# Kernel tuning notes

Measured on AMD Instinct MI355X. Metric: run time of the kernel, lower is better.

Reference implementation:

```python
import jax, jax.numpy as jnp
import numpy as np

P, L, E, D, NL, FF = 1024, 32, 512, 768, 6, 3072
H_PA, H_TR = 4, 8
VOCAB = 256


def layer_norm(x, w, b, eps=1e-5):
    mu = x.mean(-1, keepdims=True)
    var = ((x - mu) ** 2).mean(-1, keepdims=True)
    return (x - mu) / jnp.sqrt(var + eps) * w + b


def mha(x, wqkv, bqkv, wo, bo, nheads, key_mask=None):
    # x: [B,S,E]; torch nn.MultiheadAttention semantics (scale q by 1/sqrt(d))
    B, S, Emb = x.shape
    d = Emb // nheads
    qkv = x @ wqkv.T + bqkv
    q, k, v = jnp.split(qkv, 3, axis=-1)
    hd = lambda t: t.reshape(B, S, nheads, d).transpose(0, 2, 1, 3)
    q, k, v = hd(q) * (d ** -0.5), hd(k), hd(v)
    scores = jnp.einsum('bhqd,bhkd->bhqk', q, k)
    if key_mask is not None:
        scores = jnp.where(key_mask[:, None, None, :], scores, -1e9)
    a = jax.nn.softmax(scores, axis=-1)
    o = jnp.einsum('bhqk,bhkd->bhqd', a, v).transpose(0, 2, 1, 3).reshape(B, S, Emb)
    return o @ wo.T + bo


def setup_inputs() -> dict:
    key = jax.random.key(0)
    ks = jax.random.split(key, 32)
    n = lambda i, shape, s=0.02: (jax.random.normal(ks[i], shape, dtype=jnp.float32) * s)
    x = lambda i, shape: jax.random.normal(ks[i], shape, dtype=jnp.float32) * (1.0 / np.sqrt(shape[-1]))
    tokens = jax.random.randint(ks[0], (P, L), 0, VOCAB, dtype=jnp.int32)
    lengths = jax.random.randint(ks[1], (P,), 4, L + 1, dtype=jnp.int32)
    byte_emb = n(2, (VOCAB, E)).at[0].set(0.0)  # padding_idx=0
    inp = {
        'tokens': tokens, 'lengths': lengths,
        'byte_emb': byte_emb,
        'local_pos_emb': n(3, (L, E)),
        'patch_pos_emb': n(4, (P, D)),
        'pa_qkv_w': x(5, (3 * E, E)), 'pa_qkv_b': jnp.zeros((3 * E,), jnp.float32),
        'pa_out_w': x(6, (E, E)), 'pa_out_b': jnp.zeros((E,), jnp.float32),
        'proj_w': x(7, (D, E)), 'proj_b': jnp.zeros((D,), jnp.float32),
        'layers_qkv_w': x(8, (NL, 3 * D, D)), 'layers_qkv_b': jnp.zeros((NL, 3 * D), jnp.float32),
        'layers_out_w': x(9, (NL, D, D)), 'layers_out_b': jnp.zeros((NL, D), jnp.float32),
        'layers_ln1_w': jnp.ones((NL, D), jnp.float32), 'layers_ln1_b': jnp.zeros((NL, D), jnp.float32),
        'layers_ln2_w': jnp.ones((NL, D), jnp.float32), 'layers_ln2_b': jnp.zeros((NL, D), jnp.float32),
        'layers_ff1_w': x(10, (NL, FF, D)), 'layers_ff1_b': jnp.zeros((NL, FF), jnp.float32),
        'layers_ff2_w': x(11, (NL, D, FF)), 'layers_ff2_b': jnp.zeros((NL, D), jnp.float32),
        'ln_f_w': jnp.ones((D,), jnp.float32), 'ln_f_b': jnp.zeros((D,), jnp.float32),
    }
    return inp


def reference(tokens, lengths, byte_emb, local_pos_emb, patch_pos_emb,
              pa_qkv_w, pa_qkv_b, pa_out_w, pa_out_b, proj_w, proj_b,
              layers_qkv_w, layers_qkv_b, layers_out_w, layers_out_b,
              layers_ln1_w, layers_ln1_b, layers_ln2_w, layers_ln2_b,
              layers_ff1_w, layers_ff1_b, layers_ff2_w, layers_ff2_b,
              ln_f_w, ln_f_b):
    mask = jnp.arange(L) < lengths[:, None]  # [P,L] valid-byte mask
    # encode_patches: byte embed + local positions, zero padded slots
    emb = byte_emb[tokens] + local_pos_emb[None, :, :]  # [P,L,E]
    emb = emb * mask[..., None].astype(emb.dtype)
    # per-patch MHA over bytes (key padding mask), vectorized across patches
    attn = mha(emb, pa_qkv_w, pa_qkv_b, pa_out_w, pa_out_b, H_PA, key_mask=mask)
    cnt = mask.sum(-1, keepdims=True).astype(emb.dtype)
    patch_repr = (attn * mask[..., None].astype(emb.dtype)).sum(1) / cnt  # [P,E] masked mean
    # project to hidden and add patch-level positions
    h = patch_repr @ proj_w.T + proj_b + patch_pos_emb[:P]
    h = h[None]  # [1,P,D]
    # pre-norm transformer encoder, gelu FFN
    for i in range(NL):
        hn = layer_norm(h, layers_ln1_w[i], layers_ln1_b[i])
        h = h + mha(hn, layers_qkv_w[i], layers_qkv_b[i], layers_out_w[i], layers_out_b[i], H_TR)
        hn = layer_norm(h, layers_ln2_w[i], layers_ln2_b[i])
        ff = jax.nn.gelu(hn @ layers_ff1_w[i].T + layers_ff1_b[i], approximate=False)
        h = h + ff @ layers_ff2_w[i].T + layers_ff2_b[i]
    return layer_norm(h, ln_f_w, ln_f_b)[0]  # [P,D]
```

## Files before the change

### kernel.cpp

```cpp
#include <hip/hip_runtime.h>
#include <hip/hip_bf16.h>
#include <math.h>

typedef __hip_bfloat16 bf16;
typedef unsigned short u16;
typedef __attribute__((ext_vector_type(8))) short short8;
typedef __attribute__((ext_vector_type(4))) float f32x4;

#define PP 1024
#define LL 32
#define EE 512
#define DD 768
#define NLAYER 6
#define FFDIM 3072

__device__ __forceinline__ float bf2f(u16 u) { return __uint_as_float(((unsigned)u) << 16); }
__device__ __forceinline__ u16 f2b(float x) {
  unsigned u = __float_as_uint(x);
  return (u16)((u + 0x7FFFu + ((u >> 16) & 1u)) >> 16);
}

__global__ __launch_bounds__(256) void cvt4(
    const float* s0, const float* s1, const float* s2, const float* s3,
    u16* d0, u16* d1, u16* d2, u16* d3,
    int n0, int n1, int n2, int n3)
{
  int r = blockIdx.y;
  const float* s = r == 0 ? s0 : r == 1 ? s1 : r == 2 ? s2 : s3;
  u16* d        = r == 0 ? d0 : r == 1 ? d1 : r == 2 ? d2 : d3;
  int n4        = r == 0 ? n0 : r == 1 ? n1 : r == 2 ? n2 : n3;
  int i = blockIdx.x * 256 + threadIdx.x;
  if (i < n4) {
    float4 v = ((const float4*)s)[i];
    ushort4 o;
    o.x = f2b(v.x); o.y = f2b(v.y); o.z = f2b(v.z); o.w = f2b(v.w);
    ((ushort4*)d)[i] = o;
  }
}

template<bool AEMB>
__global__ __launch_bounds__(256) void gemm64(
    const bf16* A, long sAb, int lda,
    const bf16* B, long sBb, int ldb,
    float* Cf, bf16* Cb, long sCb, int ldc,
    const float* bias, int biasStride,
    const float* addf,
    int M, int N, int K, int act,
    const int* tokens, const int* lengths,
    const float* be, const float* lp)
{
  __shared__ u16 As[2][64][72];
  __shared__ u16 Bs[2][64][72];
  const int bz = blockIdx.z;
  const u16* Ap = (const u16*)A + (long)bz * sAb;
  const u16* Bp = (const u16*)B + (long)bz * sBb;
  const long coff = (long)bz * sCb;
  const int m0 = blockIdx.x << 6, n0 = blockIdx.y << 6;
  const int tid = threadIdx.x;
  const int wave = tid >> 6, lane = tid & 63;
  const int sr = tid >> 3;
  const int scc = (tid & 7) << 3;
  const int br0 = n0 + sr, br1 = n0 + sr + 32;
  const short8 zz = {0,0,0,0,0,0,0,0};
  f32x4 acc[4] = {{0.f,0.f,0.f,0.f},{0.f,0.f,0.f,0.f},{0.f,0.f,0.f,0.f},{0.f,0.f,0.f,0.f}};

#define LOADA(row, kk, dest)                                                   \
  do {                                                                         \
    if (!AEMB) {                                                               \
      dest = *(const short8*)(Ap + (long)(row) * lda + (kk));                  \
    } else {                                                                   \
      int rr = (row); int ll = rr & 31;                                        \
      if (ll < lengths[rr >> 5]) {                                             \
        const float* bpp = be + ((long)tokens[rr] << 9) + (kk);                \
        const float* lpp = lp + ((long)ll << 9) + (kk);                        \
        float4 x0 = *(const float4*)bpp, x1 = *(const float4*)(bpp + 4);       \
        float4 y0 = *(const float4*)lpp, y1 = *(const float4*)(lpp + 4);       \
        dest[0] = (short)f2b(x0.x + y0.x); dest[1] = (short)f2b(x0.y + y0.y);  \
        dest[2] = (short)f2b(x0.z + y0.z); dest[3] = (short)f2b(x0.w + y0.w);  \
        dest[4] = (short)f2b(x1.x + y1.x); dest[5] = (short)f2b(x1.y + y1.y);  \
        dest[6] = (short)f2b(x1.z + y1.z); dest[7] = (short)f2b(x1.w + y1.w);  \
      } else dest = zz;                                                        \
    }                                                                          \
  } while (0)

  {
    int ch = K < 64 ? K : 64;
    bool kv = scc < ch;
    short8 a0 = zz, a1 = zz, b0 = zz, b1 = zz;
    if (kv) {
      LOADA(m0 + sr, scc, a0);
      LOADA(m0 + sr + 32, scc, a1);
      if (br0 < N) b0 = *(const short8*)(Bp + (long)br0 * ldb + scc);
      if (br1 < N) b1 = *(const short8*)(Bp + (long)br1 * ldb + scc);
    }
    *(short8*)&As[0][sr][scc] = a0;
    *(short8*)&As[0][sr + 32][scc] = a1;
    *(short8*)&Bs[0][sr][scc] = b0;
    *(short8*)&Bs[0][sr + 32][scc] = b1;
  }
  __syncthreads();

  const int arow = (wave << 4) + (lane & 15);
  const int kq = (lane >> 4) << 3;
  int buf = 0;
  for (int k0 = 0; k0 < K; k0 += 64) {
    int knext = k0 + 64;
    bool more = knext < K;
    short8 a0 = zz, a1 = zz, b0 = zz, b1 = zz;
    if (more) {
      int ch = K - knext; if (ch > 64) ch = 64;
      bool kv = scc < ch;
      if (kv) {
        LOADA(m0 + sr, knext + scc, a0);
        LOADA(m0 + sr + 32, knext + scc, a1);
        if (br0 < N) b0 = *(const short8*)(Bp + (long)br0 * ldb + knext + scc);
        if (br1 < N) b1 = *(const short8*)(Bp + (long)br1 * ldb + knext + scc);
      }
    }
    int rem = K - k0; if (rem > 64) rem = 64;
    {
      short8 af = *(const short8*)&As[buf][arow][kq];
#pragma unroll
      for (int nt = 0; nt < 4; nt++) {
        short8 bfr = *(const short8*)&Bs[buf][(nt << 4) + (lane & 15)][kq];
        acc[nt] = __builtin_amdgcn_mfma_f32_16x16x32_bf16(af, bfr, acc[nt], 0, 0, 0);
      }
    }
    if (rem > 32) {
      short8 af = *(const short8*)&As[buf][arow][32 + kq];
#pragma unroll
      for (int nt = 0; nt < 4; nt++) {
        short8 bfr = *(const short8*)&Bs[buf][(nt << 4) + (lane & 15)][32 + kq];
        acc[nt] = __builtin_amdgcn_mfma_f32_16x16x32_bf16(af, bfr, acc[nt], 0, 0, 0);
      }
    }
    if (more) {
      int nb = buf ^ 1;
      *(short8*)&As[nb][sr][scc] = a0;
      *(short8*)&As[nb][sr + 32][scc] = a1;
      *(short8*)&Bs[nb][sr][scc] = b0;
      *(short8*)&Bs[nb][sr + 32][scc] = b1;
      __syncthreads();
      buf = nb;
    }
  }
#undef LOADA

  int rbase = m0 + (wave << 4) + ((lane >> 4) << 2);
#pragma unroll
  for (int nt = 0; nt < 4; nt++) {
    int c = n0 + (nt << 4) + (lane & 15);
    if (c >= N) continue;
    float bvl = bias ? bias[bz * biasStride + c] : 0.f;
#pragma unroll
    for (int j = 0; j < 4; j++) {
      int r = rbase + j;
      long idx = coff + (long)r * ldc + c;
      float v = acc[nt][j] + bvl;
      if (addf) v += addf[idx];
      if (act == 1) v = 0.5f * v * (1.f + erff(v * 0.70710678118654752f));
      if (Cf) Cf[idx] = v;
      if (Cb) Cb[idx] = __float2bfloat16(v);
    }
  }
}

__global__ __launch_bounds__(256) void patch_attn(
    const bf16* __restrict__ qk,
    const int* __restrict__ tokens, const int* __restrict__ lengths,
    const float* __restrict__ byte_emb, const float* __restrict__ local_pos,
    bf16* __restrict__ Z)
{
  __shared__ float wsum[4][32];
  __shared__ int tok_s[32];
  __shared__ int cnt_s;
  int p = blockIdx.x;
  int tid = threadIdx.x;
  if (tid < 32) tok_s[tid] = tokens[p * 32 + tid];
  if (tid == 0) cnt_s = lengths[p];
  __syncthreads();
  int cnt = cnt_s;
  int h = tid >> 6, lane = tid & 63;
  const u16* base = (const u16*)qk + (long)p * 32 * 1024 + h * 128;
  const int rsel = lane & 15;
  const int ksel = (lane >> 4) << 3;

  f32x4 acc[2][2] = {{{0.f,0.f,0.f,0.f},{0.f,0.f,0.f,0.f}},
                     {{0.f,0.f,0.f,0.f},{0.f,0.f,0.f,0.f}}};
#pragma unroll
  for (int kc = 0; kc < 4; kc++) {
    int ko = kc * 32 + ksel;
    short8 a0 = *(const short8*)(base + (long)rsel * 1024 + ko);
    short8 a1 = *(const short8*)(base + (long)(16 + rsel) * 1024 + ko);
    short8 b0 = *(const short8*)(base + 512 + (long)rsel * 1024 + ko);
    short8 b1 = *(const short8*)(base + 512 + (long)(16 + rsel) * 1024 + ko);
    acc[0][0] = __builtin_amdgcn_mfma_f32_16x16x32_bf16(a0, b0, acc[0][0], 0, 0, 0);
    acc[0][1] = __builtin_amdgcn_mfma_f32_16x16x32_bf16(a0, b1, acc[0][1], 0, 0, 0);
    acc[1][0] = __builtin_amdgcn_mfma_f32_16x16x32_bf16(a1, b0, acc[1][0], 0, 0, 0);
    acc[1][1] = __builtin_amdgcn_mfma_f32_16x16x32_bf16(a1, b1, acc[1][1], 0, 0, 0);
  }

  const float scale = 0.088388347648318447f;
  int j0 = lane & 15, j1 = 16 + j0;
  bool v0 = j0 < cnt, v1 = j1 < cnt;
  int rowq = (lane >> 4) << 2;
  float cs0 = 0.f, cs1 = 0.f;
#pragma unroll
  for (int ti = 0; ti < 2; ti++) {
    float s0[4], s1[4], mx[4], sm[4], e0[4], e1[4];
#pragma unroll
    for (int r = 0; r < 4; r++) {
      s0[r] = acc[ti][0][r] * scale;
      s1[r] = acc[ti][1][r] * scale;
      float a = v0 ? s0[r] : -1e30f;
      float b = v1 ? s1[r] : -1e30f;
      mx[r] = fmaxf(a, b);
    }
#pragma unroll
    for (int d = 1; d < 16; d <<= 1)
#pragma unroll
      for (int r = 0; r < 4; r++) mx[r] = fmaxf(mx[r], __shfl_xor(mx[r], d));
#pragma unroll
    for (int r = 0; r < 4; r++) {
      e0[r] = v0 ? __expf(s0[r] - mx[r]) : 0.f;
      e1[r] = v1 ? __expf(s1[r] - mx[r]) : 0.f;
      sm[r] = e0[r] + e1[r];
    }
#pragma unroll
    for (int d = 1; d < 16; d <<= 1)
#pragma unroll
      for (int r = 0; r < 4; r++) sm[r] += __shfl_xor(sm[r], d);
#pragma unroll
    for (int r = 0; r < 4; r++) {
      int row = ti * 16 + rowq + r;
      if (row < cnt) {
        float inv = 1.f / sm[r];
        cs0 += e0[r] * inv;
        cs1 += e1[r] * inv;
      }
    }
  }
  cs0 += __shfl_xor(cs0, 16); cs0 += __shfl_xor(cs0, 32);
  cs1 += __shfl_xor(cs1, 16); cs1 += __shfl_xor(cs1, 32);
  if (lane < 16) {
    float invc = 1.f / (float)cnt;
    wsum[h][lane] = cs0 * invc;
    wsum[h][16 + lane] = cs1 * invc;
  }
  __syncthreads();

  for (int e = tid; e < 512; e += 256) {
    float za0 = 0.f, za1 = 0.f, za2 = 0.f, za3 = 0.f;
    for (int j = 0; j < cnt; j++) {
      float ev = byte_emb[((long)tok_s[j] << 9) + e] + local_pos[((long)j << 9) + e];
      za0 += wsum[0][j] * ev;
      za1 += wsum[1][j] * ev;
      za2 += wsum[2][j] * ev;
      za3 += wsum[3][j] * ev;
    }
    long zb = (long)p * 2048;
    Z[zb + e]        = __float2bfloat16(za0);
    Z[zb + 512 + e]  = __float2bfloat16(za1);
    Z[zb + 1024 + e] = __float2bfloat16(za2);
    Z[zb + 1536 + e] = __float2bfloat16(za3);
  }
}

__global__ __launch_bounds__(256) void ln_kernel(
    const float* __restrict__ x, const float* __restrict__ w, const float* __restrict__ b,
    bf16* outb, float* outf, int N)
{
  __shared__ float red[8];
  __shared__ float mv[2];
  int row = blockIdx.x;
  const float* xr = x + (long)row * N;
  int tid = threadIdx.x, lane = tid & 63, wave = tid >> 6;
  float s = 0.f, s2 = 0.f;
  for (int c = tid; c < N; c += 256) { float v = xr[c]; s += v; s2 += v * v; }
  for (int o = 32; o; o >>= 1) { s += __shfl_down(s, o); s2 += __shfl_down(s2, o); }
  if (lane == 0) { red[wave] = s; red[4 + wave] = s2; }
  __syncthreads();
  if (tid == 0) {
    float ts = red[0] + red[1] + red[2] + red[3];
    float ts2 = red[4] + red[5] + red[6] + red[7];
    float mu = ts / N;
    float var = ts2 / N - mu * mu;
    mv[0] = mu; mv[1] = rsqrtf(var + 1e-5f);
  }
  __syncthreads();
  float mu = mv[0], rstd = mv[1];
  for (int c = tid; c < N; c += 256) {
    float v = (xr[c] - mu) * rstd * w[c] + b[c];
    if (outb) outb[(long)row * N + c] = __float2bfloat16(v);
    if (outf) outf[(long)row * N + c] = v;
  }
}

__global__ __launch_bounds__(256) void softmax_bf(u16* __restrict__ S)
{
  __shared__ float red[4], red2[4];
  long row = blockIdx.x;
  u16* sr = S + row * 1024;
  int tid = threadIdx.x, lane = tid & 63, wave = tid >> 6;
  const float scale = 0.10206207261596577f;
  ushort4 raw = *(const ushort4*)(sr + tid * 4);
  float v[4] = {bf2f(raw.x) * scale, bf2f(raw.y) * scale, bf2f(raw.z) * scale, bf2f(raw.w) * scale};
  float m = fmaxf(fmaxf(v[0], v[1]), fmaxf(v[2], v[3]));
  for (int o = 32; o; o >>= 1) m = fmaxf(m, __shfl_down(m, o));
  if (lane == 0) red[wave] = m;
  __syncthreads();
  m = fmaxf(fmaxf(red[0], red[1]), fmaxf(red[2], red[3]));
  float s = 0.f;
#pragma unroll
  for (int k = 0; k < 4; k++) { v[k] = __expf(v[k] - m); s += v[k]; }
  for (int o = 32; o; o >>= 1) s += __shfl_down(s, o);
  if (lane == 0) red2[wave] = s;
  __syncthreads();
  s = red2[0] + red2[1] + red2[2] + red2[3];
  float inv = 1.f / s;
  ushort4 o4;
  o4.x = f2b(v[0] * inv); o4.y = f2b(v[1] * inv); o4.z = f2b(v[2] * inv); o4.w = f2b(v[3] * inv);
  *(ushort4*)(sr + tid * 4) = o4;
}

__global__ __launch_bounds__(256) void transpose_v(
    const bf16* __restrict__ qkv, bf16* __restrict__ Vt)
{
  __shared__ u16 tile[32][33];
  int k0 = blockIdx.x << 5;
  int d0 = blockIdx.y << 5;
  int tx = threadIdx.x & 31, ty = threadIdx.x >> 5;
  const u16* q = (const u16*)qkv;
  for (int i = ty; i < 32; i += 8)
    tile[i][tx] = q[(long)(k0 + i) * 2304 + 1536 + d0 + tx];
  __syncthreads();
  u16* vt = (u16*)Vt;
  for (int i = ty; i < 32; i += 8)
    vt[(long)(d0 + i) * 1024 + k0 + tx] = tile[tx][i];
}

extern "C" void kernel_launch(void* const* d_in, const int* in_sizes, int n_in,
                              void* d_out, int out_size, void* d_ws, size_t ws_size,
                              hipStream_t stream)
{
  const int*   tokens    = (const int*)d_in[0];
  const int*   lengths   = (const int*)d_in[1];
  const float* byte_emb  = (const float*)d_in[2];
  const float* local_pos = (const float*)d_in[3];
  const float* patch_pos = (const float*)d_in[4];
  const float* pa_qkv_w  = (const float*)d_in[5];
  const float* pa_qkv_b  = (const float*)d_in[6];
  const float* pa_out_w  = (const float*)d_in[7];
  const float* pa_out_b  = (const float*)d_in[8];
  const float* proj_w    = (const float*)d_in[9];
  const float* proj_b    = (const float*)d_in[10];
  const float* Wqkv      = (const float*)d_in[11];
  const float* Bqkv      = (const float*)d_in[12];
  const float* Wout      = (const float*)d_in[13];
  const float* Bout      = (const float*)d_in[14];
  const float* ln1w      = (const float*)d_in[15];
  const float* ln1b      = (const float*)d_in[16];
  const float* ln2w      = (const float*)d_in[17];
  const float* ln2b      = (const float*)d_in[18];
  const float* W1        = (const float*)d_in[19];
  const float* B1        = (const float*)d_in[20];
  const float* W2        = (const float*)d_in[21];
  const float* B2        = (const float*)d_in[22];
  const float* lnfw      = (const float*)d_in[23];
  const float* lnfb      = (const float*)d_in[24];

  char* ws = (char*)d_ws;
  const size_t MB = 1ull << 20;
  bf16* QKC    = (bf16*)(ws);
  u16*  scores = (u16*)(ws);
  bf16* qkvt   = (bf16*)(ws + 16 * MB);
  bf16* Vt     = (bf16*)(ws + 21 * MB);
  bf16* attn   = (bf16*)(ws + 23 * MB);
  bf16* ffb    = (bf16*)(ws + 25 * MB);
  float* h     = (float*)(ws + 31 * MB);
  bf16* hn     = (bf16*)(ws + 34 * MB);
  u16*  Lw     = (u16*)(ws + 36 * MB);
  bf16* Z      = (bf16*)(ws + 64 * MB);
  bf16* o_mean = (bf16*)(ws + 68 * MB);
  bf16* t1     = (bf16*)(ws + 69 * MB);
  u16*  P1w    = (u16*)(ws + 70 * MB);

  const long oLQKV = 0;
  const long oLOUT = 1769472;
  const long oLW1  = 2359296;
  const long oLW2  = 4718592;
  const long oPAQ  = 0;
  const long oPAO  = 786432;
  const long oPRJ  = 1048576;

  cvt4<<<dim3(768, 3), 256, 0, stream>>>(
      pa_qkv_w, pa_out_w, proj_w, nullptr,
      P1w + oPAQ, P1w + oPAO, P1w + oPRJ, nullptr,
      786432 / 4, 262144 / 4, 393216 / 4, 0);
  gemm64<true><<<dim3(512, 16, 1), 256, 0, stream>>>(
      nullptr, 0, 0, (bf16*)(P1w + oPAQ), 0, EE, nullptr, QKC, 0, 1024,
      pa_qkv_b, 0, nullptr, 32768, 1024, EE, 0,
      tokens, lengths, byte_emb, local_pos);
  patch_attn<<<PP, 256, 0, stream>>>(
      QKC, tokens, lengths, byte_emb, local_pos, Z);
  gemm64<false><<<dim3(16, 2, 4), 256, 0, stream>>>(
      Z, 512, 2048, (bf16*)(P1w + oPAQ + 1024L * EE), 128L * EE, EE,
      nullptr, o_mean, 128, EE, pa_qkv_b + 1024, 128, nullptr, PP, 128, EE, 0,
      nullptr, nullptr, nullptr, nullptr);
  gemm64<false><<<dim3(16, 8, 1), 256, 0, stream>>>(
      o_mean, 0, EE, (bf16*)(P1w + oPAO), 0, EE, nullptr, t1, 0, EE,
      pa_out_b, 0, nullptr, PP, EE, EE, 0,
      nullptr, nullptr, nullptr, nullptr);
  gemm64<false><<<dim3(16, 12, 1), 256, 0, stream>>>(
      t1, 0, EE, (bf16*)(P1w + oPRJ), 0, EE, h, nullptr, 0, DD,
      proj_b, 0, patch_pos, PP, DD, EE, 0,
      nullptr, nullptr, nullptr, nullptr);

  for (int i = 0; i < NLAYER; i++) {
    cvt4<<<dim3(2304, 4), 256, 0, stream>>>(
        Wqkv + (long)i * 2304 * DD, Wout + (long)i * DD * DD,
        W1 + (long)i * FFDIM * DD, W2 + (long)i * DD * FFDIM,
        Lw + oLQKV, Lw + oLOUT, Lw + oLW1, Lw + oLW2,
        1769472 / 4, 589824 / 4, 2359296 / 4, 2359296 / 4);
    ln_kernel<<<PP, 256, 0, stream>>>(h, ln1w + i * DD, ln1b + i * DD, hn, nullptr, DD);
    gemm64<false><<<dim3(16, 36, 1), 256, 0, stream>>>(
        hn, 0, DD, (bf16*)(Lw + oLQKV), 0, DD, nullptr, qkvt, 0, 2304,
        Bqkv + i * 2304, 0, nullptr, PP, 2304, DD, 0,
        nullptr, nullptr, nullptr, nullptr);
    gemm64<false><<<dim3(16, 16, 8), 256, 0, stream>>>(
        qkvt, 96, 2304, qkvt + DD, 96, 2304, nullptr, (bf16*)scores, 1024L * 1024, 1024,
        nullptr, 0, nullptr, 1024, 1024, 96, 0,
        nullptr, nullptr, nullptr, nullptr);
    softmax_bf<<<8192, 256, 0, stream>>>(scores);
    transpose_v<<<dim3(32, 24), 256, 0, stream>>>(qkvt, Vt);
    gemm64<false><<<dim3(16, 2, 8), 256, 0, stream>>>(
        (bf16*)scores, 1024L * 1024, 1024, Vt, 96L * 1024, 1024, nullptr, attn, 96, DD,
        nullptr, 0, nullptr, 1024, 96, 1024, 0,
        nullptr, nullptr, nullptr, nullptr);
    gemm64<false><<<dim3(16, 12, 1), 256, 0, stream>>>(
        attn, 0, DD, (bf16*)(Lw + oLOUT), 0, DD, h, nullptr, 0, DD,
        Bout + i * DD, 0, h, PP, DD, DD, 0,
        nullptr, nullptr, nullptr, nullptr);
    ln_kernel<<<PP, 256, 0, stream>>>(h, ln2w + i * DD, ln2b + i * DD, hn, nullptr, DD);
    gemm64<false><<<dim3(16, 48, 1), 256, 0, stream>>>(
        hn, 0, DD, (bf16*)(Lw + oLW1), 0, DD, nullptr, ffb, 0, FFDIM,
        B1 + i * FFDIM, 0, nullptr, PP, FFDIM, DD, 1,
        nullptr, nullptr, nullptr, nullptr);
    gemm64<false><<<dim3(16, 12, 1), 256, 0, stream>>>(
        ffb, 0, FFDIM, (bf16*)(Lw + oLW2), 0, FFDIM, h, nullptr, 0, DD,
        B2 + i * DD, 0, h, PP, DD, FFDIM, 0,
        nullptr, nullptr, nullptr, nullptr);
  }
  ln_kernel<<<PP, 256, 0, stream>>>(h, lnfw, lnfb, nullptr, (float*)d_out, DD);
}
```

Before: 1.216 ms.

## Fuse transformer attention into flash kernel and chunk patch-attention QK projection

Replaces the per-layer score GEMM, separate softmax, and PV GEMM with a single online-softmax flash attention kernel. This avoids writing and re-reading the 8x1024x1024 bf16 score matrix every layer. The patch stage now materializes embeddings in a separate kernel and runs the QK projection with a new 128x128-tile GEMM in four chunks of 256 patches, so the QKC buffer stays small and likely cache-resident. The flash kernel launches only 128 blocks and reads K directly from global memory without shared-memory staging, which may limit occupancy and bandwidth.

```diff
diff --git a/kernel.cpp b/kernel.cpp
--- a/kernel.cpp
+++ b/kernel.cpp
@@ -38,16 +38,95 @@
   }
 }
 
-template<bool AEMB>
+__global__ __launch_bounds__(256) void embed_kernel(
+    const int* __restrict__ tokens, const int* __restrict__ lengths,
+    const float* __restrict__ byte_emb, const float* __restrict__ local_pos,
+    bf16* __restrict__ emb)
+{
+  int pl = blockIdx.x;
+  int p = pl >> 5, l = pl & 31;
+  bool valid = l < lengths[p];
+  int tok = tokens[pl];
+  const float* be = byte_emb + (long)tok * EE;
+  const float* lp = local_pos + (long)l * EE;
+  u16* out = (u16*)emb + (long)pl * EE;
+  for (int e = threadIdx.x; e < EE; e += 256) {
+    float v = valid ? be[e] + lp[e] : 0.f;
+    out[e] = f2b(v);
+  }
+}
+
+__global__ __launch_bounds__(256) void gemm128(
+    const bf16* A, int lda, const bf16* B, int ldb,
+    float* Cf, bf16* Cb, int ldc, const float* bias, int K)
+{
+  __shared__ u16 As[128][40];
+  __shared__ u16 Bs[128][40];
+  const int m0 = blockIdx.x << 7, n0 = blockIdx.y << 7;
+  const int tid = threadIdx.x;
+  const int wave = tid >> 6, lane = tid & 63;
+  const int sr = tid >> 1;
+  const int sc = (tid & 1) << 4;
+  const u16* Ap = (const u16*)A;
+  const u16* Bp = (const u16*)B;
+  const int wr = (wave & 1) << 6;
+  const int wc = (wave >> 1) << 6;
+  const int fr = lane & 15;
+  const int kq = (lane >> 4) << 3;
+  f32x4 acc[4][4];
+#pragma unroll
+  for (int i = 0; i < 4; i++)
+#pragma unroll
+    for (int j = 0; j < 4; j++) acc[i][j] = (f32x4){0.f, 0.f, 0.f, 0.f};
+
+  for (int k0 = 0; k0 < K; k0 += 32) {
+    short8 a0 = *(const short8*)(Ap + (long)(m0 + sr) * lda + k0 + sc);
+    short8 a1 = *(const short8*)(Ap + (long)(m0 + sr) * lda + k0 + sc + 8);
+    short8 b0 = *(const short8*)(Bp + (long)(n0 + sr) * ldb + k0 + sc);
+    short8 b1 = *(const short8*)(Bp + (long)(n0 + sr) * ldb + k0 + sc + 8);
+    __syncthreads();
+    *(short8*)&As[sr][sc] = a0;
+    *(short8*)&As[sr][sc + 8] = a1;
+    *(short8*)&Bs[sr][sc] = b0;
+    *(short8*)&Bs[sr][sc + 8] = b1;
+    __syncthreads();
+    short8 af[4], bfv[4];
+#pragma unroll
+    for (int i = 0; i < 4; i++) af[i] = *(const short8*)&As[wr + i * 16 + fr][kq];
+#pragma unroll
+    for (int j = 0; j < 4; j++) bfv[j] = *(const short8*)&Bs[wc + j * 16 + fr][kq];
+#pragma unroll
+    for (int i = 0; i < 4; i++)
+#pragma unroll
+      for (int j = 0; j < 4; j++)
+        acc[i][j] = __builtin_amdgcn_mfma_f32_16x16x32_bf16(af[i], bfv[j], acc[i][j], 0, 0, 0);
+  }
+  const int rq = (lane >> 4) << 2;
+#pragma unroll
+  for (int j = 0; j < 4; j++) {
+    int c = n0 + wc + j * 16 + fr;
+    float bvl = bias ? bias[c] : 0.f;
+#pragma unroll
+    for (int i = 0; i < 4; i++) {
+#pragma unroll
+      for (int r = 0; r < 4; r++) {
+        int row = m0 + wr + i * 16 + rq + r;
+        long idx = (long)row * ldc + c;
+        float v = acc[i][j][r] + bvl;
+        if (Cf) Cf[idx] = v;
+        if (Cb) Cb[idx] = __float2bfloat16(v);
+      }
+    }
+  }
+}
+
 __global__ __launch_bounds__(256) void gemm64(
     const bf16* A, long sAb, int lda,
     const bf16* B, long sBb, int ldb,
     float* Cf, bf16* Cb, long sCb, int ldc,
     const float* bias, int biasStride,
     const float* addf,
-    int M, int N, int K, int act,
-    const int* tokens, const int* lengths,
-    const float* be, const float* lp)
+    int M, int N, int K, int act)
 {
   __shared__ u16 As[2][64][72];
   __shared__ u16 Bs[2][64][72];
@@ -64,32 +143,13 @@
   const short8 zz = {0,0,0,0,0,0,0,0};
   f32x4 acc[4] = {{0.f,0.f,0.f,0.f},{0.f,0.f,0.f,0.f},{0.f,0.f,0.f,0.f},{0.f,0.f,0.f,0.f}};
 
-#define LOADA(row, kk, dest)                                                   \
-  do {                                                                         \
-    if (!AEMB) {                                                               \
-      dest = *(const short8*)(Ap + (long)(row) * lda + (kk));                  \
-    } else {                                                                   \
-      int rr = (row); int ll = rr & 31;                                        \
-      if (ll < lengths[rr >> 5]) {                                             \
-        const float* bpp = be + ((long)tokens[rr] << 9) + (kk);                \
-        const float* lpp = lp + ((long)ll << 9) + (kk);                        \
-        float4 x0 = *(const float4*)bpp, x1 = *(const float4*)(bpp + 4);       \
-        float4 y0 = *(const float4*)lpp, y1 = *(const float4*)(lpp + 4);       \
-        dest[0] = (short)f2b(x0.x + y0.x); dest[1] = (short)f2b(x0.y + y0.y);  \
-        dest[2] = (short)f2b(x0.z + y0.z); dest[3] = (short)f2b(x0.w + y0.w);  \
-        dest[4] = (short)f2b(x1.x + y1.x); dest[5] = (short)f2b(x1.y + y1.y);  \
-        dest[6] = (short)f2b(x1.z + y1.z); dest[7] = (short)f2b(x1.w + y1.w);  \
-      } else dest = zz;                                                        \
-    }                                                                          \
-  } while (0)
-
   {
     int ch = K < 64 ? K : 64;
     bool kv = scc < ch;
     short8 a0 = zz, a1 = zz, b0 = zz, b1 = zz;
     if (kv) {
-      LOADA(m0 + sr, scc, a0);
-      LOADA(m0 + sr + 32, scc, a1);
+      a0 = *(const short8*)(Ap + (long)(m0 + sr) * lda + scc);
+      a1 = *(const short8*)(Ap + (long)(m0 + sr + 32) * lda + scc);
       if (br0 < N) b0 = *(const short8*)(Bp + (long)br0 * ldb + scc);
       if (br1 < N) b1 = *(const short8*)(Bp + (long)br1 * ldb + scc);
     }
@@ -111,8 +171,8 @@
       int ch = K - knext; if (ch > 64) ch = 64;
       bool kv = scc < ch;
       if (kv) {
-        LOADA(m0 + sr, knext + scc, a0);
-        LOADA(m0 + sr + 32, knext + scc, a1);
+        a0 = *(const short8*)(Ap + (long)(m0 + sr) * lda + knext + scc);
+        a1 = *(const short8*)(Ap + (long)(m0 + sr + 32) * lda + knext + scc);
         if (br0 < N) b0 = *(const short8*)(Bp + (long)br0 * ldb + knext + scc);
         if (br1 < N) b1 = *(const short8*)(Bp + (long)br1 * ldb + knext + scc);
       }
@@ -144,7 +204,6 @@
       buf = nb;
     }
   }
-#undef LOADA
 
   int rbase = m0 + (wave << 4) + ((lane >> 4) << 2);
 #pragma unroll
@@ -162,6 +221,111 @@
       if (Cf) Cf[idx] = v;
       if (Cb) Cb[idx] = __float2bfloat16(v);
     }
+  }
+}
+
+__global__ __launch_bounds__(256) void attn_flash(
+    const bf16* __restrict__ qkvt,
+    const bf16* __restrict__ Vt,
+    bf16* __restrict__ attn)
+{
+  __shared__ u16 Pls[2][4][16][64];
+  const int q0 = blockIdx.x << 6;
+  const int h = blockIdx.y;
+  const int tid = threadIdx.x, wave = tid >> 6, lane = tid & 63;
+  const u16* qp = (const u16*)qkvt;
+  const u16* vp = (const u16*)Vt + (long)h * 96 * 1024;
+  const int fr = lane & 15;
+  const int kq = (lane >> 4) << 3;
+  const int rq = (lane >> 4) << 2;
+  const int qrow = q0 + wave * 16 + fr;
+  short8 qf[3];
+#pragma unroll
+  for (int c = 0; c < 3; c++)
+    qf[c] = *(const short8*)(qp + (long)qrow * 2304 + h * 96 + c * 32 + kq);
+  f32x4 O[6];
+#pragma unroll
+  for (int ct = 0; ct < 6; ct++) O[ct] = (f32x4){0.f, 0.f, 0.f, 0.f};
+  float mrun[4] = {-1e30f, -1e30f, -1e30f, -1e30f};
+  float lrun[4] = {0.f, 0.f, 0.f, 0.f};
+  const float scale = 0.10206207261596577f;
+
+  for (int kt = 0; kt < 16; kt++) {
+    const int k0 = kt << 6;
+    f32x4 S[4];
+#pragma unroll
+    for (int j = 0; j < 4; j++) S[j] = (f32x4){0.f, 0.f, 0.f, 0.f};
+#pragma unroll
+    for (int c = 0; c < 3; c++) {
+#pragma unroll
+      for (int j = 0; j < 4; j++) {
+        short8 kf = *(const short8*)(qp + (long)(k0 + j * 16 + fr) * 2304 + 768 + h * 96 + c * 32 + kq);
+        S[j] = __builtin_amdgcn_mfma_f32_16x16x32_bf16(qf[c], kf, S[j], 0, 0, 0);
+      }
+    }
+    float mx[4];
+#pragma unroll
+    for (int r = 0; r < 4; r++) {
+      float m = -1e30f;
+#pragma unroll
+      for (int j = 0; j < 4; j++) { S[j][r] *= scale; m = fmaxf(m, S[j][r]); }
+      mx[r] = m;
+    }
+#pragma unroll
+    for (int d = 1; d < 16; d <<= 1)
+#pragma unroll
+      for (int r = 0; r < 4; r++) mx[r] = fmaxf(mx[r], __shfl_xor(mx[r], d));
+    float alpha[4];
+#pragma unroll
+    for (int r = 0; r < 4; r++) {
+      float mn = fmaxf(mrun[r], mx[r]);
+      alpha[r] = __expf(mrun[r] - mn);
+      mrun[r] = mn;
+    }
+    float rs[4] = {0.f, 0.f, 0.f, 0.f};
+#pragma unroll
+    for (int j = 0; j < 4; j++)
+#pragma unroll
+      for (int r = 0; r < 4; r++) {
+        float e = __expf(S[j][r] - mrun[r]);
+        S[j][r] = e;
+        rs[r] += e;
+      }
+#pragma unroll
+    for (int d = 1; d < 16; d <<= 1)
+#pragma unroll
+      for (int r = 0; r < 4; r++) rs[r] += __shfl_xor(rs[r], d);
+#pragma unroll
+    for (int r = 0; r < 4; r++) lrun[r] = lrun[r] * alpha[r] + rs[r];
+#pragma unroll
+    for (int ct = 0; ct < 6; ct++)
+#pragma unroll
+      for (int r = 0; r < 4; r++) O[ct][r] *= alpha[r];
+    const int pb = kt & 1;
+#pragma unroll
+    for (int j = 0; j < 4; j++)
+#pragma unroll
+      for (int r = 0; r < 4; r++)
+        Pls[pb][wave][rq + r][j * 16 + fr] = f2b(S[j][r]);
+    __syncthreads();
+#pragma unroll
+    for (int kc = 0; kc < 2; kc++) {
+      short8 pa = *(const short8*)&Pls[pb][wave][fr][kc * 32 + kq];
+#pragma unroll
+      for (int ct = 0; ct < 6; ct++) {
+        short8 vf = *(const short8*)(vp + (long)(ct * 16 + fr) * 1024 + k0 + kc * 32 + kq);
+        O[ct] = __builtin_amdgcn_mfma_f32_16x16x32_bf16(pa, vf, O[ct], 0, 0, 0);
+      }
+    }
+  }
+  u16* op = (u16*)attn;
+#pragma unroll
+  for (int r = 0; r < 4; r++) {
+    float inv = 1.f / lrun[r];
+    int row = q0 + wave * 16 + rq + r;
+#pragma unroll
+    for (int ct = 0; ct < 6; ct++)
+      op[(long)row * 768 + h * 96 + ct * 16 + fr] = f2b(O[ct][r] * inv);
   }
 }
 
@@ -294,33 +458,6 @@
     if (outb) outb[(long)row * N + c] = __float2bfloat16(v);
     if (outf) outf[(long)row * N + c] = v;
   }
-}
-
-__global__ __launch_bounds__(256) void softmax_bf(u16* __restrict__ S)
-{
-  __shared__ float red[4], red2[4];
-  long row = blockIdx.x;
-  u16* sr = S + row * 1024;
-  int tid = threadIdx.x, lane = tid & 63, wave = tid >> 6;
-  const float scale = 0.10206207261596577f;
-  ushort4 raw = *(const ushort4*)(sr + tid * 4);
-  float v[4] = {bf2f(raw.x) * scale, bf2f(raw.y) * scale, bf2f(raw.z) * scale, bf2f(raw.w) * scale};
-  float m = fmaxf(fmaxf(v[0], v[1]), fmaxf(v[2], v[3]));
-  for (int o = 32; o; o >>= 1) m = fmaxf(m, __shfl_down(m, o));
-  if (lane == 0) red[wave] = m;
-  __syncthreads();
-  m = fmaxf(fmaxf(red[0], red[1]), fmaxf(red[2], red[3]));
-  float s = 0.f;
-#pragma unroll
-  for (int k = 0; k < 4; k++) { v[k] = __expf(v[k] - m); s += v[k]; }
-  for (int o = 32; o; o >>= 1) s += __shfl_down(s, o);
-  if (lane == 0) red2[wave] = s;
-  __syncthreads();
-  s = red2[0] + red2[1] + red2[2] + red2[3];
-  float inv = 1.f / s;
-  ushort4 o4;
-  o4.x = f2b(v[0] * inv); o4.y = f2b(v[1] * inv); o4.z = f2b(v[2] * inv); o4.w = f2b(v[3] * inv);
-  *(ushort4*)(sr + tid * 4) = o4;
 }
 
 __global__ __launch_bounds__(256) void transpose_v(
@@ -372,18 +509,18 @@
   char* ws = (char*)d_ws;
   const size_t MB = 1ull << 20;
   bf16* QKC    = (bf16*)(ws);
-  u16*  scores = (u16*)(ws);
-  bf16* qkvt   = (bf16*)(ws + 16 * MB);
-  bf16* Vt     = (bf16*)(ws + 21 * MB);
-  bf16* attn   = (bf16*)(ws + 23 * MB);
-  bf16* ffb    = (bf16*)(ws + 25 * MB);
-  float* h     = (float*)(ws + 31 * MB);
-  bf16* hn     = (bf16*)(ws + 34 * MB);
-  u16*  Lw     = (u16*)(ws + 36 * MB);
-  bf16* Z      = (bf16*)(ws + 64 * MB);
-  bf16* o_mean = (bf16*)(ws + 68 * MB);
-  bf16* t1     = (bf16*)(ws + 69 * MB);
-  u16*  P1w    = (u16*)(ws + 70 * MB);
+  bf16* embC   = (bf16*)(ws + 16 * MB);
+  bf16* Z      = (bf16*)(ws + 24 * MB);
+  bf16* o_mean = (bf16*)(ws + 28 * MB);
+  bf16* t1     = (bf16*)(ws + 29 * MB);
+  u16*  P1w    = (u16*)(ws + 30 * MB);
+  float* h     = (float*)(ws + 33 * MB);
+  bf16* hn     = (bf16*)(ws + 36 * MB);
+  bf16* qkvt   = (bf16*)(ws + 38 * MB);
+  bf16* Vt     = (bf16*)(ws + 43 * MB);
+  bf16* attn   = (bf16*)(ws + 45 * MB);
+  bf16* ffb    = (bf16*)(ws + 47 * MB);
+  u16*  Lw     = (u16*)(ws + 53 * MB);
 
   const long oLQKV = 0;
   const long oLOUT = 1769472;
@@ -397,24 +534,24 @@
       pa_qkv_w, pa_out_w, proj_w, nullptr,
       P1w + oPAQ, P1w + oPAO, P1w + oPRJ, nullptr,
       786432 / 4, 262144 / 4, 393216 / 4, 0);
-  gemm64<true><<<dim3(512, 16, 1), 256, 0, stream>>>(
-      nullptr, 0, 0, (bf16*)(P1w + oPAQ), 0, EE, nullptr, QKC, 0, 1024,
-      pa_qkv_b, 0, nullptr, 32768, 1024, EE, 0,
-      tokens, lengths, byte_emb, local_pos);
-  patch_attn<<<PP, 256, 0, stream>>>(
-      QKC, tokens, lengths, byte_emb, local_pos, Z);
-  gemm64<false><<<dim3(16, 2, 4), 256, 0, stream>>>(
+  for (int c = 0; c < 4; c++) {
+    int p0 = c * 256, row0 = c * 8192;
+    embed_kernel<<<8192, 256, 0, stream>>>(
+        tokens + row0, lengths + p0, byte_emb, local_pos, embC);
+    gemm128<<<dim3(64, 8), 256, 0, stream>>>(
+        embC, EE, (bf16*)(P1w + oPAQ), EE, nullptr, QKC, 1024, pa_qkv_b, EE);
+    patch_attn<<<256, 256, 0, stream>>>(
+        QKC, tokens + row0, lengths + p0, byte_emb, local_pos, Z + (long)p0 * 2048);
+  }
+  gemm64<<<dim3(16, 2, 4), 256, 0, stream>>>(
       Z, 512, 2048, (bf16*)(P1w + oPAQ + 1024L * EE), 128L * EE, EE,
-      nullptr, o_mean, 128, EE, pa_qkv_b + 1024, 128, nullptr, PP, 128, EE, 0,
-      nullptr, nullptr, nullptr, nullptr);
-  gemm64<false><<<dim3(16, 8, 1), 256, 0, stream>>>(
+      nullptr, o_mean, 128, EE, pa_qkv_b + 1024, 128, nullptr, PP, 128, EE, 0);
+  gemm64<<<dim3(16, 8, 1), 256, 0, stream>>>(
       o_mean, 0, EE, (bf16*)(P1w + oPAO), 0, EE, nullptr, t1, 0, EE,
-      pa_out_b, 0, nullptr, PP, EE, EE, 0,
-      nullptr, nullptr, nullptr, nullptr);
-  gemm64<false><<<dim3(16, 12, 1), 256, 0, stream>>>(
+      pa_out_b, 0, nullptr, PP, EE, EE, 0);
+  gemm64<<<dim3(16, 12, 1), 256, 0, stream>>>(
       t1, 0, EE, (bf16*)(P1w + oPRJ), 0, EE, h, nullptr, 0, DD,
-      proj_b, 0, patch_pos, PP, DD, EE, 0,
-      nullptr, nullptr, nullptr, nullptr);
+      proj_b, 0, patch_pos, PP, DD, EE, 0);
 
   for (int i = 0; i < NLAYER; i++) {
     cvt4<<<dim3(2304, 4), 256, 0, stream>>>(
@@ -423,33 +560,21 @@
         Lw + oLQKV, Lw + oLOUT, Lw + oLW1, Lw + oLW2,
         1769472 / 4, 589824 / 4, 2359296 / 4, 2359296 / 4);
     ln_kernel<<<PP, 256, 0, stream>>>(h, ln1w + i * DD, ln1b + i * DD, hn, nullptr, DD);
-    gemm64<false><<<dim3(16, 36, 1), 256, 0, stream>>>(
+    gemm64<<<dim3(16, 36, 1), 256, 0, stream>>>(
         hn, 0, DD, (bf16*)(Lw + oLQKV), 0, DD, nullptr, qkvt, 0, 2304,
-        Bqkv + i * 2304, 0, nullptr, PP, 2304, DD, 0,
-        nullptr, nullptr, nullptr, nullptr);
-    gemm64<false><<<dim3(16, 16, 8), 256, 0, stream>>>(
-        qkvt, 96, 2304, qkvt + DD, 96, 2304, nullptr, (bf16*)scores, 1024L * 1024, 1024,
-        nullptr, 0, nullptr, 1024, 1024, 96, 0,
-        nullptr, nullptr, nullptr, nullptr);
-    softmax_bf<<<8192, 256, 0, stream>>>(scores);
+        Bqkv + i * 2304, 0, nullptr, PP, 2304, DD, 0);
     transpose_v<<<dim3(32, 24), 256, 0, stream>>>(qkvt, Vt);
-    gemm64<false><<<dim3(16, 2, 8), 256, 0, stream>>>(
-        (bf16*)scores, 1024L * 1024, 1024, Vt, 96L * 1024, 1024, nullptr, attn, 96, DD,
-        nullptr, 0, nullptr, 1024, 96, 1024, 0,
-        nullptr, nullptr, nullptr, nullptr);
-    gemm64<false><<<dim3(16, 12, 1), 256, 0, stream>>>(
+    attn_flash<<<dim3(16, 8), 256, 0, stream>>>(qkvt, Vt, attn);
+    gemm64<<<dim3(16, 12, 1), 256, 0, stream>>>(
         attn, 0, DD, (bf16*)(Lw + oLOUT), 0, DD, h, nullptr, 0, DD,
-        Bout + i * DD, 0, h, PP, DD, DD, 0,
-        nullptr, nullptr, nullptr, nullptr);
+        Bout + i * DD, 0, h, PP, DD, DD, 0);
     ln_kernel<<<PP, 256, 0, stream>>>(h, ln2w + i * DD, ln2b + i * DD, hn, nullptr, DD);
-    gemm64<false><<<dim3(16, 48, 1), 256, 0, stream>>>(
+    gemm64<<<dim3(16, 48, 1), 256, 0, stream>>>(
         hn, 0, DD, (bf16*)(Lw + oLW1), 0, DD, nullptr, ffb, 0, FFDIM,
-        B1 + i * FFDIM, 0, nullptr, PP, FFDIM, DD, 1,
-        nullptr, nullptr, nullptr, nullptr);
-    gemm64<false><<<dim3(16, 12, 1), 256, 0, stream>>>(
+        B1 + i * FFDIM, 0, nullptr, PP, FFDIM, DD, 1);
+    gemm64<<<dim3(16, 12, 1), 256, 0, stream>>>(
         ffb, 0, FFDIM, (bf16*)(Lw + oLW2), 0, FFDIM, h, nullptr, 0, DD,
-        B2 + i * DD, 0, h, PP, DD, FFDIM, 0,
-        nullptr, nullptr, nullptr, nullptr);
+        B2 + i * DD, 0, h, PP, DD, FFDIM, 0);
   }
   ln_kernel<<<PP, 256, 0, stream>>>(h, lnfw, lnfb, nullptr, (float*)d_out, DD);
 }
```

Result: slower. 1.506 ms (+23.8%).
